# Kernel optimization log

Hardware: AMD Instinct MI355X
Metric: run time of the kernel (lower is better)

The kernel has to match this reference:

```python
import jax, jax.numpy as jnp
import numpy as np

B, N, H, W = 128, 8192, 7, 7


def setup_inputs() -> dict:
    key = jax.random.key(0)
    ks = jax.random.split(key, 10)
    inp = {
        'x': jax.random.normal(ks[0], (B, N, H, W), dtype=jnp.float32),
        'y': jax.random.normal(ks[1], (B, N), dtype=jnp.float32),
        # nn.MultiheadAttention(embed_dim=1, num_heads=1) params (all scalar)
        'wq': jax.random.normal(ks[2], (), dtype=jnp.float32),
        'wk': jax.random.normal(ks[3], (), dtype=jnp.float32),
        'wv': jax.random.normal(ks[4], (), dtype=jnp.float32),
        'bq': jax.random.normal(ks[5], (), dtype=jnp.float32) * 0.1,
        'bk': jax.random.normal(ks[6], (), dtype=jnp.float32) * 0.1,
        'bv': jax.random.normal(ks[7], (), dtype=jnp.float32) * 0.1,
        'wo': jax.random.normal(ks[8], (), dtype=jnp.float32),
        'bo': jax.random.normal(ks[9], (), dtype=jnp.float32) * 0.1,
    }
    return inp


def _mha1(q_src, kv_src, wq, bq, wk, bk, wv, bv, wo, bo):
    # embed_dim=1, num_heads=1, scale = 1/sqrt(1) = 1.
    # torch sees (seq=B, batch=N, embed=1): attention mixes the B axis per n.
    q = q_src * wq + bq            # [B, N]
    k = kv_src * wk + bk           # [B, N]
    v = kv_src * wv + bv           # [B, N]
    scores = jnp.einsum('in,jn->ijn', q, k)      # [B, B, N]
    a = jax.nn.softmax(scores, axis=1)           # softmax over keys j
    out = jnp.einsum('ijn,jn->in', a, v)         # [B, N]
    return out * wo + bo


def reference(x, y, wq, bq, wk, bk, wv, bv, wo, bo):
    xp = jnp.mean(x, axis=(2, 3))                # AdaptiveAvgPool2d((1,1)) -> [B, N]
    self_x = _mha1(xp, xp, wq, bq, wk, bk, wv, bv, wo, bo)
    self_y = _mha1(y, y, wq, bq, wk, bk, wv, bv, wo, bo)
    cross_x = _mha1(xp, y, wq, bq, wk, bk, wv, bv, wo, bo)
    cross_y = _mha1(y, xp, wq, bq, wk, bk, wv, bv, wo, bo)
    f_x = xp + self_x
    f_y = y + self_y
    c_f_x = cross_x + f_x
    c_f_y = cross_y + f_y
    return jnp.concatenate((c_f_x, c_f_y), axis=1)   # [B, 2N]
```

## Files before the change

### kernel.cpp

```cpp
#include <hip/hip_runtime.h>


constexpr int B_SEQ = 128;
constexpr int N_COL = 8192;
constexpr int HWP   = 49;
constexpr int NT    = 256;
constexpr int TC    = 4;
constexpr int VSTR  = 132;
constexpr int OSTR  = 5;

typedef float v2f __attribute__((ext_vector_type(2)));

#if __has_builtin(__builtin_elementwise_fma)
#define VFMA(a, b, c) __builtin_elementwise_fma((a), (b), (c))
#else
__device__ __forceinline__ v2f VFMA(v2f a, v2f b, v2f c) {
    v2f r; r.x = fmaf(a.x, b.x, c.x); r.y = fmaf(a.y, b.y, c.y); return r;
}
#endif

__global__ __launch_bounds__(NT, 5) void rsca_fused(
    const float* __restrict__ x, const float* __restrict__ y,
    const float* __restrict__ pwq, const float* __restrict__ pwk,
    const float* __restrict__ pwv, const float* __restrict__ pbq,
    const float* __restrict__ pbk, const float* __restrict__ pbv,
    const float* __restrict__ pwo, const float* __restrict__ pbo,
    float* __restrict__ out)
{
    __shared__ float xv[TC * VSTR];
    __shared__ float yv[TC * VSTR];
    __shared__ float pmnx[8][TC], pmxx[8][TC];
    __shared__ float pmny[4][TC], pmxy[4][TC];
    __shared__ float obuf[2][B_SEQ * OSTR];

    const int t    = threadIdx.x;
    const int bid  = blockIdx.x;
    const int cg = (bid & 7) * ((N_COL / TC) >> 3) + (bid >> 3);
    const int n0 = cg * TC;

    const int ql   = t & 3;
    const int seg  = t >> 2;
    const int lane = t & 63;
    const int wid  = t >> 6;

    const float wq = pwq[0], wk = pwk[0], wv = pwv[0];
    const float bq = pbq[0], bk = pbk[0], bv = pbv[0];
    const float wo = pwo[0], bo = pbo[0];
    const float L2E = 1.4426950408889634f;
    const float wkL = wk * L2E, bkL = bk * L2E;
    const float alpha = wo * wv;
    const float beta2 = 2.0f * (wo * bv + bo);

    {
        const int j = t >> 2, c = t & 3;
        const float fy0 = y[(size_t)j * N_COL + n0 + c];
        const float fy1 = y[(size_t)(j + 64) * N_COL + n0 + c];
        yv[c * VSTR + j]      = fy0;
        yv[c * VSTR + j + 64] = fy1;
        float mn = fminf(fy0, fy1), mx = fmaxf(fy0, fy1);
        #pragma unroll
        for (int off = 4; off <= 32; off <<= 1) {
            mn = fminf(mn, __shfl_xor(mn, off));
            mx = fmaxf(mx, __shfl_xor(mx, off));
        }
        if (lane < 4) { pmny[wid][lane] = mn; pmxy[wid][lane] = mx; }
    }

    for (int pass = 0; pass < 2; ++pass) {
        const int j = pass * 64 + seg;
        const float4* __restrict__ base =
            (const float4*)(x + ((size_t)j * N_COL + n0) * (size_t)HWP);
        float4 v[13];
        #pragma unroll
        for (int k = 0; k < 12; ++k) v[k] = base[ql + 4 * k];
        v[12] = base[48];

        float s0 = 0.f, s1 = 0.f, s2 = 0.f, s3 = 0.f;
        s0 += v[0].x + v[0].y + v[0].z + v[0].w;
        s0 += v[1].x + v[1].y + v[1].z + v[1].w;
        s0 += v[2].x + v[2].y + v[2].z + v[2].w;
        s1 += v[4].x + v[4].y + v[4].z + v[4].w;
        s1 += v[5].x + v[5].y + v[5].z + v[5].w;
        s2 += v[7].x + v[7].y + v[7].z + v[7].w;
        s2 += v[8].x + v[8].y + v[8].z + v[8].w;
        s3 += v[10].x + v[10].y + v[10].z + v[10].w;
        s3 += v[11].x + v[11].y + v[11].z + v[11].w;
        { const float sm = v[3].x + v[3].y + v[3].z + v[3].w;
          const float cr = (ql == 0) ? v[3].x : 0.0f;
          s0 += cr; s1 += sm - cr; }
        { const float sm = v[6].x + v[6].y + v[6].z + v[6].w;
          const float cr = (ql == 0) ? (v[6].x + v[6].y) : 0.0f;
          s1 += cr; s2 += sm - cr; }
        { const float sm = v[9].x + v[9].y + v[9].z + v[9].w;
          const float cr = (ql == 0) ? (v[9].x + v[9].y + v[9].z) : 0.0f;
          s2 += cr; s3 += sm - cr; }
        const float tail = v[12].x + v[12].y + v[12].z + v[12].w;

        s0 += __shfl_xor(s0, 1); s1 += __shfl_xor(s1, 1);
        s2 += __shfl_xor(s2, 1); s3 += __shfl_xor(s3, 1);
        s0 += __shfl_xor(s0, 2); s1 += __shfl_xor(s1, 2);
        s2 += __shfl_xor(s2, 2); s3 += __shfl_xor(s3, 2);
        float r = s0;
        r = (ql == 1) ? s1 : r;
        r = (ql == 2) ? s2 : r;
        r = (ql == 3) ? (s3 + tail) : r;
        const float mean = r * (1.0f / HWP);
        xv[ql * VSTR + j] = mean;

        float mn = mean, mx = mean;
        #pragma unroll
        for (int off = 4; off <= 32; off <<= 1) {
            mn = fminf(mn, __shfl_xor(mn, off));
            mx = fmaxf(mx, __shfl_xor(mx, off));
        }
        if (lane < 4) {
            pmnx[pass * 4 + wid][lane] = mn;
            pmxx[pass * 4 + wid][lane] = mx;
        }
    }
    __syncthreads();

    const int i  = t & (B_SEQ - 1);
    const int ch = t >> 7;
    #pragma unroll
    for (int cc = 0; cc < 2; ++cc) {
        const int c = ch * 2 + cc;
        const float* __restrict__ vx = &xv[c * VSTR];
        const float* __restrict__ vy = &yv[c * VSTR];

        float vxmn = pmnx[0][c], vxmx = pmxx[0][c];
        #pragma unroll
        for (int s = 1; s < 8; ++s) {
            vxmn = fminf(vxmn, pmnx[s][c]);
            vxmx = fmaxf(vxmx, pmxx[s][c]);
        }
        float vymn = pmny[0][c], vymx = pmxy[0][c];
        #pragma unroll
        for (int s = 1; s < 4; ++s) {
            vymn = fminf(vymn, pmny[s][c]);
            vymx = fmaxf(vymx, pmxy[s][c]);
        }
        const float axv = fmaf(vxmx, wkL, bkL), bxv = fmaf(vxmn, wkL, bkL);
        const float kxmx = fmaxf(axv, bxv), kxmn = fminf(axv, bxv);
        const float ayv = fmaf(vymx, wkL, bkL), byv = fmaf(vymn, wkL, bkL);
        const float kymx = fmaxf(ayv, byv), kymn = fminf(ayv, byv);

        const float xi = vx[i], yi = vy[i];
        const float qx = fmaf(xi, wq, bq), qy = fmaf(yi, wq, bq);
        const float nmsx = -(qx >= 0.f ? qx * kxmx : qx * kxmn);
        const float nmcy = -(qy >= 0.f ? qy * kxmx : qy * kxmn);
        const float nmsy = -(qy >= 0.f ? qy * kymx : qy * kymn);
        const float nmcx = -(qx >= 0.f ? qx * kymx : qx * kymn);

        const float qxw = qx * wkL, qyw = qy * wkL;
        const v2f qxw2 = {qxw, qxw}, qyw2 = {qyw, qyw};
        const float csx = fmaf(qx, bkL, nmsx), ccy = fmaf(qy, bkL, nmcy);
        const float csy = fmaf(qy, bkL, nmsy), ccx = fmaf(qx, bkL, nmcx);
        const v2f csx2 = {csx, csx}, ccy2 = {ccy, ccy};
        const v2f csy2 = {csy, csy}, ccx2 = {ccx, ccx};

        v2f s0sx = {0.f, 0.f}, s1sx = {0.f, 0.f};
        v2f s0cy = {0.f, 0.f}, s1cy = {0.f, 0.f};
        v2f s0sy = {0.f, 0.f}, s1sy = {0.f, 0.f};
        v2f s0cx = {0.f, 0.f}, s1cx = {0.f, 0.f};

        auto px2 = [&](float v0, float v1) {
            const v2f vvj = {v0, v1};
            v2f t1 = VFMA(qxw2, vvj, csx2);
            v2f e1; e1.x = __builtin_amdgcn_exp2f(t1.x);
                    e1.y = __builtin_amdgcn_exp2f(t1.y);
            s1sx = VFMA(e1, vvj, s1sx); s0sx += e1;
            v2f t2 = VFMA(qyw2, vvj, ccy2);
            v2f e2; e2.x = __builtin_amdgcn_exp2f(t2.x);
                    e2.y = __builtin_amdgcn_exp2f(t2.y);
            s1cy = VFMA(e2, vvj, s1cy); s0cy += e2;
        };
        auto py2 = [&](float v0, float v1) {
            const v2f vvj = {v0, v1};
            v2f t3 = VFMA(qyw2, vvj, csy2);
            v2f e3; e3.x = __builtin_amdgcn_exp2f(t3.x);
                    e3.y = __builtin_amdgcn_exp2f(t3.y);
            s1sy = VFMA(e3, vvj, s1sy); s0sy += e3;
            v2f t4 = VFMA(qxw2, vvj, ccx2);
            v2f e4; e4.x = __builtin_amdgcn_exp2f(t4.x);
                    e4.y = __builtin_amdgcn_exp2f(t4.y);
            s1cx = VFMA(e4, vvj, s1cx); s0cx += e4;
        };

        float4 a0 = *(const float4*)&vx[0], a1 = *(const float4*)&vx[4];
        float4 b0 = *(const float4*)&vy[0], b1 = *(const float4*)&vy[4];
        for (int j0 = 0; j0 < B_SEQ; j0 += 8) {
            const int jn = (j0 + 8) & (B_SEQ - 1);
            float4 na0 = *(const float4*)&vx[jn];
            float4 na1 = *(const float4*)&vx[jn + 4];
            float4 nb0 = *(const float4*)&vy[jn];
            float4 nb1 = *(const float4*)&vy[jn + 4];

            px2(a0.x, a0.y); px2(a0.z, a0.w); px2(a1.x, a1.y); px2(a1.z, a1.w);
            py2(b0.x, b0.y); py2(b0.z, b0.w); py2(b1.x, b1.y); py2(b1.z, b1.w);

            a0 = na0; a1 = na1; b0 = nb0; b1 = nb1;
        }
        const float S0sx = s0sx.x + s0sx.y, S1sx = s1sx.x + s1sx.y;
        const float S0cy = s0cy.x + s0cy.y, S1cy = s1cy.x + s1cy.y;
        const float S0sy = s0sy.x + s0sy.y, S1sy = s1sy.x + s1sy.y;
        const float S0cx = s0cx.x + s0cx.y, S1cx = s1cx.x + s1cx.y;
        const float mx_attn = S1sx * __builtin_amdgcn_rcpf(S0sx)
                            + S1cx * __builtin_amdgcn_rcpf(S0cx);
        const float my_attn = S1sy * __builtin_amdgcn_rcpf(S0sy)
                            + S1cy * __builtin_amdgcn_rcpf(S0cy);
        obuf[0][i * OSTR + c] = fmaf(alpha, mx_attn, beta2 + xi);
        obuf[1][i * OSTR + c] = fmaf(alpha, my_attn, beta2 + yi);
    }
    __syncthreads();

    {
        const int set = t >> 7;
        const int ii  = t & (B_SEQ - 1);
        const float* p = &obuf[set][ii * OSTR];
        float4 val;
        val.x = p[0]; val.y = p[1]; val.z = p[2]; val.w = p[3];
        *(float4*)&out[(size_t)ii * (2 * N_COL) + (size_t)set * N_COL + n0] = val;
    }
}

extern "C" void kernel_launch(void* const* d_in, const int* in_sizes, int n_in,
                              void* d_out, int out_size, void* d_ws, size_t ws_size,
                              hipStream_t stream) {
    const float* x   = (const float*)d_in[0];
    const float* y   = (const float*)d_in[1];
    const float* pwq = (const float*)d_in[2];
    const float* pwk = (const float*)d_in[3];
    const float* pwv = (const float*)d_in[4];
    const float* pbq = (const float*)d_in[5];
    const float* pbk = (const float*)d_in[6];
    const float* pbv = (const float*)d_in[7];
    const float* pwo = (const float*)d_in[8];
    const float* pbo = (const float*)d_in[9];
    float* out = (float*)d_out;

    rsca_fused<<<dim3(N_COL / TC), dim3(NT), 0, stream>>>(
        x, y, pwq, pwk, pwv, pbq, pbk, pbv, pwo, pbo, out);
}
```

Before: 322.9 us.

## Overlap x pooling with y-only attention via block-parity phase staggering

Blocks are split by parity. Even blocks pool x first, as before. Odd blocks first compute the y self-attention, which needs only y, then pool x and finish the three x-dependent attentions. This staggers the memory-heavy pooling phase against the exp-heavy compute phase across co-resident blocks, so bandwidth and ALU are used at the same time. The attention loops are also restructured to process two columns at once per phase, with partial results kept in shared memory. This can raise register pressure, and the odd blocks take an extra barrier.

Result: faster. 316.6 us (-2.0%).

```diff
diff --git a/kernel.cpp b/kernel.cpp
--- a/kernel.cpp
+++ b/kernel.cpp
@@ -37,6 +37,7 @@
     const int bid  = blockIdx.x;
     const int cg = (bid & 7) * ((N_COL / TC) >> 3) + (bid >> 3);
     const int n0 = cg * TC;
+    const int par = (bid >> 8) & 1;
 
     const int ql   = t & 3;
     const int seg  = t >> 2;
@@ -66,151 +67,223 @@
         if (lane < 4) { pmny[wid][lane] = mn; pmxy[wid][lane] = mx; }
     }
 
-    for (int pass = 0; pass < 2; ++pass) {
-        const int j = pass * 64 + seg;
-        const float4* __restrict__ base =
-            (const float4*)(x + ((size_t)j * N_COL + n0) * (size_t)HWP);
-        float4 v[13];
-        #pragma unroll
-        for (int k = 0; k < 12; ++k) v[k] = base[ql + 4 * k];
-        v[12] = base[48];
-
-        float s0 = 0.f, s1 = 0.f, s2 = 0.f, s3 = 0.f;
-        s0 += v[0].x + v[0].y + v[0].z + v[0].w;
-        s0 += v[1].x + v[1].y + v[1].z + v[1].w;
-        s0 += v[2].x + v[2].y + v[2].z + v[2].w;
-        s1 += v[4].x + v[4].y + v[4].z + v[4].w;
-        s1 += v[5].x + v[5].y + v[5].z + v[5].w;
-        s2 += v[7].x + v[7].y + v[7].z + v[7].w;
-        s2 += v[8].x + v[8].y + v[8].z + v[8].w;
-        s3 += v[10].x + v[10].y + v[10].z + v[10].w;
-        s3 += v[11].x + v[11].y + v[11].z + v[11].w;
-        { const float sm = v[3].x + v[3].y + v[3].z + v[3].w;
-          const float cr = (ql == 0) ? v[3].x : 0.0f;
-          s0 += cr; s1 += sm - cr; }
-        { const float sm = v[6].x + v[6].y + v[6].z + v[6].w;
-          const float cr = (ql == 0) ? (v[6].x + v[6].y) : 0.0f;
-          s1 += cr; s2 += sm - cr; }
-        { const float sm = v[9].x + v[9].y + v[9].z + v[9].w;
-          const float cr = (ql == 0) ? (v[9].x + v[9].y + v[9].z) : 0.0f;
-          s2 += cr; s3 += sm - cr; }
-        const float tail = v[12].x + v[12].y + v[12].z + v[12].w;
-
-        s0 += __shfl_xor(s0, 1); s1 += __shfl_xor(s1, 1);
-        s2 += __shfl_xor(s2, 1); s3 += __shfl_xor(s3, 1);
-        s0 += __shfl_xor(s0, 2); s1 += __shfl_xor(s1, 2);
-        s2 += __shfl_xor(s2, 2); s3 += __shfl_xor(s3, 2);
-        float r = s0;
-        r = (ql == 1) ? s1 : r;
-        r = (ql == 2) ? s2 : r;
-        r = (ql == 3) ? (s3 + tail) : r;
-        const float mean = r * (1.0f / HWP);
-        xv[ql * VSTR + j] = mean;
-
-        float mn = mean, mx = mean;
-        #pragma unroll
-        for (int off = 4; off <= 32; off <<= 1) {
-            mn = fminf(mn, __shfl_xor(mn, off));
-            mx = fmaxf(mx, __shfl_xor(mx, off));
-        }
-        if (lane < 4) {
-            pmnx[pass * 4 + wid][lane] = mn;
-            pmxx[pass * 4 + wid][lane] = mx;
-        }
-    }
-    __syncthreads();
+    auto pool_x = [&]() {
+        for (int pass = 0; pass < 2; ++pass) {
+            const int j = pass * 64 + seg;
+            const float4* __restrict__ base =
+                (const float4*)(x + ((size_t)j * N_COL + n0) * (size_t)HWP);
+            float4 v[13];
+            #pragma unroll
+            for (int k = 0; k < 12; ++k) v[k] = base[ql + 4 * k];
+            v[12] = base[48];
+
+            float s0 = 0.f, s1 = 0.f, s2 = 0.f, s3 = 0.f;
+            s0 += v[0].x + v[0].y + v[0].z + v[0].w;
+            s0 += v[1].x + v[1].y + v[1].z + v[1].w;
+            s0 += v[2].x + v[2].y + v[2].z + v[2].w;
+            s1 += v[4].x + v[4].y + v[4].z + v[4].w;
+            s1 += v[5].x + v[5].y + v[5].z + v[5].w;
+            s2 += v[7].x + v[7].y + v[7].z + v[7].w;
+            s2 += v[8].x + v[8].y + v[8].z + v[8].w;
+            s3 += v[10].x + v[10].y + v[10].z + v[10].w;
+            s3 += v[11].x + v[11].y + v[11].z + v[11].w;
+            { const float sm = v[3].x + v[3].y + v[3].z + v[3].w;
+              const float cr = (ql == 0) ? v[3].x : 0.0f;
+              s0 += cr; s1 += sm - cr; }
+            { const float sm = v[6].x + v[6].y + v[6].z + v[6].w;
+              const float cr = (ql == 0) ? (v[6].x + v[6].y) : 0.0f;
+              s1 += cr; s2 += sm - cr; }
+            { const float sm = v[9].x + v[9].y + v[9].z + v[9].w;
+              const float cr = (ql == 0) ? (v[9].x + v[9].y + v[9].z) : 0.0f;
+              s2 += cr; s3 += sm - cr; }
+            const float tail = v[12].x + v[12].y + v[12].z + v[12].w;
+
+            s0 += __shfl_xor(s0, 1); s1 += __shfl_xor(s1, 1);
+            s2 += __shfl_xor(s2, 1); s3 += __shfl_xor(s3, 1);
+            s0 += __shfl_xor(s0, 2); s1 += __shfl_xor(s1, 2);
+            s2 += __shfl_xor(s2, 2); s3 += __shfl_xor(s3, 2);
+            float r = s0;
+            r = (ql == 1) ? s1 : r;
+            r = (ql == 2) ? s2 : r;
+            r = (ql == 3) ? (s3 + tail) : r;
+            const float mean = r * (1.0f / HWP);
+            xv[ql * VSTR + j] = mean;
+
+            float mn = mean, mx = mean;
+            #pragma unroll
+            for (int off = 4; off <= 32; off <<= 1) {
+                mn = fminf(mn, __shfl_xor(mn, off));
+                mx = fmaxf(mx, __shfl_xor(mx, off));
+            }
+            if (lane < 4) {
+                pmnx[pass * 4 + wid][lane] = mn;
+                pmxx[pass * 4 + wid][lane] = mx;
+            }
+        }
+    };
 
     const int i  = t & (B_SEQ - 1);
     const int ch = t >> 7;
+    const int c0 = ch * 2, c1 = ch * 2 + 1;
+    const float* __restrict__ vx0 = &xv[c0 * VSTR];
+    const float* __restrict__ vx1 = &xv[c1 * VSTR];
+    const float* __restrict__ vy0 = &yv[c0 * VSTR];
+    const float* __restrict__ vy1 = &yv[c1 * VSTR];
+    float* const po0y = &obuf[1][i * OSTR + c0];
+    float* const po1y = &obuf[1][i * OSTR + c1];
+    float* const po0x = &obuf[0][i * OSTR + c0];
+    float* const po1x = &obuf[0][i * OSTR + c1];
+
+    auto PAIR = [&](v2f& s0, v2f& s1, const v2f& qw, const v2f& cs,
+                    float u0, float u1) {
+        v2f vv = {u0, u1};
+        v2f tt = VFMA(qw, vv, cs);
+        v2f e; e.x = __builtin_amdgcn_exp2f(tt.x);
+               e.y = __builtin_amdgcn_exp2f(tt.y);
+        s1 = VFMA(e, vv, s1); s0 += e;
+    };
+
+    if (par == 0) pool_x();
+    __syncthreads();
+
+    float vymn0 = pmny[0][c0], vymx0 = pmxy[0][c0];
+    float vymn1 = pmny[0][c1], vymx1 = pmxy[0][c1];
     #pragma unroll
-    for (int cc = 0; cc < 2; ++cc) {
-        const int c = ch * 2 + cc;
-        const float* __restrict__ vx = &xv[c * VSTR];
-        const float* __restrict__ vy = &yv[c * VSTR];
-
-        float vxmn = pmnx[0][c], vxmx = pmxx[0][c];
-        #pragma unroll
-        for (int s = 1; s < 8; ++s) {
-            vxmn = fminf(vxmn, pmnx[s][c]);
-            vxmx = fmaxf(vxmx, pmxx[s][c]);
-        }
-        float vymn = pmny[0][c], vymx = pmxy[0][c];
-        #pragma unroll
-        for (int s = 1; s < 4; ++s) {
-            vymn = fminf(vymn, pmny[s][c]);
-            vymx = fmaxf(vymx, pmxy[s][c]);
-        }
-        const float axv = fmaf(vxmx, wkL, bkL), bxv = fmaf(vxmn, wkL, bkL);
-        const float kxmx = fmaxf(axv, bxv), kxmn = fminf(axv, bxv);
-        const float ayv = fmaf(vymx, wkL, bkL), byv = fmaf(vymn, wkL, bkL);
-        const float kymx = fmaxf(ayv, byv), kymn = fminf(ayv, byv);
-
-        const float xi = vx[i], yi = vy[i];
-        const float qx = fmaf(xi, wq, bq), qy = fmaf(yi, wq, bq);
-        const float nmsx = -(qx >= 0.f ? qx * kxmx : qx * kxmn);
-        const float nmcy = -(qy >= 0.f ? qy * kxmx : qy * kxmn);
-        const float nmsy = -(qy >= 0.f ? qy * kymx : qy * kymn);
-        const float nmcx = -(qx >= 0.f ? qx * kymx : qx * kymn);
-
-        const float qxw = qx * wkL, qyw = qy * wkL;
-        const v2f qxw2 = {qxw, qxw}, qyw2 = {qyw, qyw};
-        const float csx = fmaf(qx, bkL, nmsx), ccy = fmaf(qy, bkL, nmcy);
-        const float csy = fmaf(qy, bkL, nmsy), ccx = fmaf(qx, bkL, nmcx);
-        const v2f csx2 = {csx, csx}, ccy2 = {ccy, ccy};
-        const v2f csy2 = {csy, csy}, ccx2 = {ccx, ccx};
-
-        v2f s0sx = {0.f, 0.f}, s1sx = {0.f, 0.f};
-        v2f s0cy = {0.f, 0.f}, s1cy = {0.f, 0.f};
-        v2f s0sy = {0.f, 0.f}, s1sy = {0.f, 0.f};
-        v2f s0cx = {0.f, 0.f}, s1cx = {0.f, 0.f};
-
-        auto px2 = [&](float v0, float v1) {
-            const v2f vvj = {v0, v1};
-            v2f t1 = VFMA(qxw2, vvj, csx2);
-            v2f e1; e1.x = __builtin_amdgcn_exp2f(t1.x);
-                    e1.y = __builtin_amdgcn_exp2f(t1.y);
-            s1sx = VFMA(e1, vvj, s1sx); s0sx += e1;
-            v2f t2 = VFMA(qyw2, vvj, ccy2);
-            v2f e2; e2.x = __builtin_amdgcn_exp2f(t2.x);
-                    e2.y = __builtin_amdgcn_exp2f(t2.y);
-            s1cy = VFMA(e2, vvj, s1cy); s0cy += e2;
-        };
-        auto py2 = [&](float v0, float v1) {
-            const v2f vvj = {v0, v1};
-            v2f t3 = VFMA(qyw2, vvj, csy2);
-            v2f e3; e3.x = __builtin_amdgcn_exp2f(t3.x);
-                    e3.y = __builtin_amdgcn_exp2f(t3.y);
-            s1sy = VFMA(e3, vvj, s1sy); s0sy += e3;
-            v2f t4 = VFMA(qxw2, vvj, ccx2);
-            v2f e4; e4.x = __builtin_amdgcn_exp2f(t4.x);
-                    e4.y = __builtin_amdgcn_exp2f(t4.y);
-            s1cx = VFMA(e4, vvj, s1cx); s0cx += e4;
-        };
-
-        float4 a0 = *(const float4*)&vx[0], a1 = *(const float4*)&vx[4];
-        float4 b0 = *(const float4*)&vy[0], b1 = *(const float4*)&vy[4];
+    for (int s = 1; s < 4; ++s) {
+        vymn0 = fminf(vymn0, pmny[s][c0]); vymx0 = fmaxf(vymx0, pmxy[s][c0]);
+        vymn1 = fminf(vymn1, pmny[s][c1]); vymx1 = fmaxf(vymx1, pmxy[s][c1]);
+    }
+    const float ay0 = fmaf(vymx0, wkL, bkL), by0 = fmaf(vymn0, wkL, bkL);
+    const float kymx0 = fmaxf(ay0, by0), kymn0 = fminf(ay0, by0);
+    const float ay1 = fmaf(vymx1, wkL, bkL), by1 = fmaf(vymn1, wkL, bkL);
+    const float kymx1 = fmaxf(ay1, by1), kymn1 = fminf(ay1, by1);
+
+    const float yi0 = vy0[i], yi1 = vy1[i];
+    const float qy0 = fmaf(yi0, wq, bq), qy1 = fmaf(yi1, wq, bq);
+
+    {
+        const float nm0 = -(qy0 >= 0.f ? qy0 * kymx0 : qy0 * kymn0);
+        const float nm1 = -(qy1 >= 0.f ? qy1 * kymx1 : qy1 * kymn1);
+        const float qw0 = qy0 * wkL, qw1 = qy1 * wkL;
+        const v2f qw20 = {qw0, qw0}, qw21 = {qw1, qw1};
+        const float cs0 = fmaf(qy0, bkL, nm0), cs1 = fmaf(qy1, bkL, nm1);
+        const v2f cs20 = {cs0, cs0}, cs21 = {cs1, cs1};
+
+        v2f s00 = {0.f, 0.f}, s10 = {0.f, 0.f};
+        v2f s01 = {0.f, 0.f}, s11 = {0.f, 0.f};
         for (int j0 = 0; j0 < B_SEQ; j0 += 8) {
-            const int jn = (j0 + 8) & (B_SEQ - 1);
-            float4 na0 = *(const float4*)&vx[jn];
-            float4 na1 = *(const float4*)&vx[jn + 4];
-            float4 nb0 = *(const float4*)&vy[jn];
-            float4 nb1 = *(const float4*)&vy[jn + 4];
-
-            px2(a0.x, a0.y); px2(a0.z, a0.w); px2(a1.x, a1.y); px2(a1.z, a1.w);
-            py2(b0.x, b0.y); py2(b0.z, b0.w); py2(b1.x, b1.y); py2(b1.z, b1.w);
-
-            a0 = na0; a1 = na1; b0 = nb0; b1 = nb1;
-        }
-        const float S0sx = s0sx.x + s0sx.y, S1sx = s1sx.x + s1sx.y;
-        const float S0cy = s0cy.x + s0cy.y, S1cy = s1cy.x + s1cy.y;
-        const float S0sy = s0sy.x + s0sy.y, S1sy = s1sy.x + s1sy.y;
-        const float S0cx = s0cx.x + s0cx.y, S1cx = s1cx.x + s1cx.y;
-        const float mx_attn = S1sx * __builtin_amdgcn_rcpf(S0sx)
-                            + S1cx * __builtin_amdgcn_rcpf(S0cx);
-        const float my_attn = S1sy * __builtin_amdgcn_rcpf(S0sy)
-                            + S1cy * __builtin_amdgcn_rcpf(S0cy);
-        obuf[0][i * OSTR + c] = fmaf(alpha, mx_attn, beta2 + xi);
-        obuf[1][i * OSTR + c] = fmaf(alpha, my_attn, beta2 + yi);
+            const float4 p00 = *(const float4*)&vy0[j0];
+            const float4 p01 = *(const float4*)&vy0[j0 + 4];
+            const float4 p10 = *(const float4*)&vy1[j0];
+            const float4 p11 = *(const float4*)&vy1[j0 + 4];
+            PAIR(s00, s10, qw20, cs20, p00.x, p00.y);
+            PAIR(s01, s11, qw21, cs21, p10.x, p10.y);
+            PAIR(s00, s10, qw20, cs20, p00.z, p00.w);
+            PAIR(s01, s11, qw21, cs21, p10.z, p10.w);
+            PAIR(s00, s10, qw20, cs20, p01.x, p01.y);
+            PAIR(s01, s11, qw21, cs21, p11.x, p11.y);
+            PAIR(s00, s10, qw20, cs20, p01.z, p01.w);
+            PAIR(s01, s11, qw21, cs21, p11.z, p11.w);
+        }
+        *po0y = (s10.x + s10.y) * __builtin_amdgcn_rcpf(s00.x + s00.y);
+        *po1y = (s11.x + s11.y) * __builtin_amdgcn_rcpf(s01.x + s01.y);
+    }
+
+    if (par == 1) { pool_x(); __syncthreads(); }
+
+    float vxmn0 = pmnx[0][c0], vxmx0 = pmxx[0][c0];
+    float vxmn1 = pmnx[0][c1], vxmx1 = pmxx[0][c1];
+    #pragma unroll
+    for (int s = 1; s < 8; ++s) {
+        vxmn0 = fminf(vxmn0, pmnx[s][c0]); vxmx0 = fmaxf(vxmx0, pmxx[s][c0]);
+        vxmn1 = fminf(vxmn1, pmnx[s][c1]); vxmx1 = fmaxf(vxmx1, pmxx[s][c1]);
+    }
+    const float ax0 = fmaf(vxmx0, wkL, bkL), bx0 = fmaf(vxmn0, wkL, bkL);
+    const float kxmx0 = fmaxf(ax0, bx0), kxmn0 = fminf(ax0, bx0);
+    const float ax1 = fmaf(vxmx1, wkL, bkL), bx1 = fmaf(vxmn1, wkL, bkL);
+    const float kxmx1 = fmaxf(ax1, bx1), kxmn1 = fminf(ax1, bx1);
+
+    const float xi0 = vx0[i], xi1 = vx1[i];
+    const float qx0 = fmaf(xi0, wq, bq), qx1 = fmaf(xi1, wq, bq);
+
+    {
+        const float nms0 = -(qx0 >= 0.f ? qx0 * kxmx0 : qx0 * kxmn0);
+        const float nms1 = -(qx1 >= 0.f ? qx1 * kxmx1 : qx1 * kxmn1);
+        const float nmc0 = -(qy0 >= 0.f ? qy0 * kxmx0 : qy0 * kxmn0);
+        const float nmc1 = -(qy1 >= 0.f ? qy1 * kxmx1 : qy1 * kxmn1);
+        const float qwx0 = qx0 * wkL, qwx1 = qx1 * wkL;
+        const float qwy0 = qy0 * wkL, qwy1 = qy1 * wkL;
+        const v2f qwx20 = {qwx0, qwx0}, qwx21 = {qwx1, qwx1};
+        const v2f qwy20 = {qwy0, qwy0}, qwy21 = {qwy1, qwy1};
+        const float csa0 = fmaf(qx0, bkL, nms0), csa1 = fmaf(qx1, bkL, nms1);
+        const float csb0 = fmaf(qy0, bkL, nmc0), csb1 = fmaf(qy1, bkL, nmc1);
+        const v2f csa20 = {csa0, csa0}, csa21 = {csa1, csa1};
+        const v2f csb20 = {csb0, csb0}, csb21 = {csb1, csb1};
+
+        v2f sa00 = {0.f, 0.f}, sa10 = {0.f, 0.f};
+        v2f sb00 = {0.f, 0.f}, sb10 = {0.f, 0.f};
+        v2f sa01 = {0.f, 0.f}, sa11 = {0.f, 0.f};
+        v2f sb01 = {0.f, 0.f}, sb11 = {0.f, 0.f};
+        for (int j0 = 0; j0 < B_SEQ; j0 += 8) {
+            const float4 p00 = *(const float4*)&vx0[j0];
+            const float4 p01 = *(const float4*)&vx0[j0 + 4];
+            const float4 p10 = *(const float4*)&vx1[j0];
+            const float4 p11 = *(const float4*)&vx1[j0 + 4];
+            PAIR(sa00, sa10, qwx20, csa20, p00.x, p00.y);
+            PAIR(sb00, sb10, qwy20, csb20, p00.x, p00.y);
+            PAIR(sa01, sa11, qwx21, csa21, p10.x, p10.y);
+            PAIR(sb01, sb11, qwy21, csb21, p10.x, p10.y);
+            PAIR(sa00, sa10, qwx20, csa20, p00.z, p00.w);
+            PAIR(sb00, sb10, qwy20, csb20, p00.z, p00.w);
+            PAIR(sa01, sa11, qwx21, csa21, p10.z, p10.w);
+            PAIR(sb01, sb11, qwy21, csb21, p10.z, p10.w);
+            PAIR(sa00, sa10, qwx20, csa20, p01.x, p01.y);
+            PAIR(sb00, sb10, qwy20, csb20, p01.x, p01.y);
+            PAIR(sa01, sa11, qwx21, csa21, p11.x, p11.y);
+            PAIR(sb01, sb11, qwy21, csb21, p11.x, p11.y);
+            PAIR(sa00, sa10, qwx20, csa20, p01.z, p01.w);
+            PAIR(sb00, sb10, qwy20, csb20, p01.z, p01.w);
+            PAIR(sa01, sa11, qwx21, csa21, p11.z, p11.w);
+            PAIR(sb01, sb11, qwy21, csb21, p11.z, p11.w);
+        }
+        const float sx0 = (sa10.x + sa10.y) * __builtin_amdgcn_rcpf(sa00.x + sa00.y);
+        const float sx1 = (sa11.x + sa11.y) * __builtin_amdgcn_rcpf(sa01.x + sa01.y);
+        const float cy0 = (sb10.x + sb10.y) * __builtin_amdgcn_rcpf(sb00.x + sb00.y);
+        const float cy1 = (sb11.x + sb11.y) * __builtin_amdgcn_rcpf(sb01.x + sb01.y);
+        *po0y = fmaf(alpha, *po0y + cy0, beta2 + yi0);
+        *po1y = fmaf(alpha, *po1y + cy1, beta2 + yi1);
+        *po0x = sx0;
+        *po1x = sx1;
+    }
+
+    {
+        const float nm0 = -(qx0 >= 0.f ? qx0 * kymx0 : qx0 * kymn0);
+        const float nm1 = -(qx1 >= 0.f ? qx1 * kymx1 : qx1 * kymn1);
+        const float qw0 = qx0 * wkL, qw1 = qx1 * wkL;
+        const v2f qw20 = {qw0, qw0}, qw21 = {qw1, qw1};
+        const float cs0 = fmaf(qx0, bkL, nm0), cs1 = fmaf(qx1, bkL, nm1);
+        const v2f cs20 = {cs0, cs0}, cs21 = {cs1, cs1};
+
+        v2f s00 = {0.f, 0.f}, s10 = {0.f, 0.f};
+        v2f s01 = {0.f, 0.f}, s11 = {0.f, 0.f};
+        for (int j0 = 0; j0 < B_SEQ; j0 += 8) {
+            const float4 p00 = *(const float4*)&vy0[j0];
+            const float4 p01 = *(const float4*)&vy0[j0 + 4];
+            const float4 p10 = *(const float4*)&vy1[j0];
+            const float4 p11 = *(const float4*)&vy1[j0 + 4];
+            PAIR(s00, s10, qw20, cs20, p00.x, p00.y);
+            PAIR(s01, s11, qw21, cs21, p10.x, p10.y);
+            PAIR(s00, s10, qw20, cs20, p00.z, p00.w);
+            PAIR(s01, s11, qw21, cs21, p10.z, p10.w);
+            PAIR(s00, s10, qw20, cs20, p01.x, p01.y);
+            PAIR(s01, s11, qw21, cs21, p11.x, p11.y);
+            PAIR(s00, s10, qw20, cs20, p01.z, p01.w);
+            PAIR(s01, s11, qw21, cs21, p11.z, p11.w);
+        }
+        const float cx0 = (s10.x + s10.y) * __builtin_amdgcn_rcpf(s00.x + s00.y);
+        const float cx1 = (s11.x + s11.y) * __builtin_amdgcn_rcpf(s01.x + s01.y);
+        *po0x = fmaf(alpha, *po0x + cx0, beta2 + xi0);
+        *po1x = fmaf(alpha, *po1x + cx1, beta2 + xi1);
     }
     __syncthreads();
 
```
